# Performance work log

Measured on AMD Instinct MI355X. Metric: run time of the kernel, lower is better.

Reference implementation:

```python
import jax, jax.numpy as jnp
import numpy as np

DT = 1e-3
STEPS = 128
UNITS_OSC = 512
MLP_UNITS = [1024, 512, 256]
ACTION_DIM = 256
BATCH = 64


def setup_inputs() -> dict:
    key = jax.random.key(0)
    ks = jax.random.split(key, 16)
    inp = {
        "z": jax.random.normal(ks[0], (BATCH, 2 * UNITS_OSC), dtype=jnp.float32),
        "omega": jax.random.uniform(ks[1], (BATCH, 1), dtype=jnp.float32),
        "b": jax.random.uniform(ks[2], (BATCH, UNITS_OSC), dtype=jnp.float32),
    }
    dims = [UNITS_OSC] + MLP_UNITS
    i = 3
    for l, (din, dout) in enumerate(zip(dims[:-1], dims[1:])):
        scale = 1.0 / np.sqrt(din)
        inp[f"W{l}_re"] = (jax.random.normal(ks[i], (din, dout), dtype=jnp.float32) * scale); i += 1
        inp[f"W{l}_im"] = (jax.random.normal(ks[i], (din, dout), dtype=jnp.float32) * scale); i += 1
        inp[f"b{l}_re"] = jnp.zeros((dout,), dtype=jnp.float32)
        inp[f"b{l}_im"] = jnp.zeros((dout,), dtype=jnp.float32)
    return inp


def _hopf(z, omega, b):
    # z: (B, 2*U) = [real | imag]; Hopf dynamics with harmonic frequencies k*omega
    x, y = z[:, :UNITS_OSC], z[:, UNITS_OSC:]
    r2 = x * x + y * y
    w = omega * jnp.arange(1, UNITS_OSC + 1, dtype=z.dtype)  # (B, U)
    dx = (b - r2) * x - w * y
    dy = (b - r2) * y + w * x
    return jnp.concatenate([x + DT * dx, y + DT * dy], axis=-1)


def _complex_mlp(z, params):
    # complex dense stack: (xr+i*yi) @ (Wr+i*Wi) + (br+i*bi), tanh on re/im parts
    x, y = jnp.split(z, 2, axis=-1)
    for (Wr, Wi, br, bi) in params:
        xr = x @ Wr - y @ Wi + br
        yi = x @ Wi + y @ Wr + bi
        x, y = jnp.tanh(xr), jnp.tanh(yi)
    return jnp.concatenate([x, y], axis=-1)


def reference(z, omega, b,
              W0_re, W0_im, b0_re, b0_im,
              W1_re, W1_im, b1_re, b1_im,
              W2_re, W2_im, b2_re, b2_im):
    params = [(W0_re, W0_im, b0_re, b0_im),
              (W1_re, W1_im, b1_re, b1_im),
              (W2_re, W2_im, b2_re, b2_im)]
    # first oscillator step (done before the while_loop in the original)
    z1 = _hopf(z, omega, b)
    o0 = _complex_mlp(z1, params)

    def step(zc, _):
        zn = _hopf(zc, omega, b)
        return zn, _complex_mlp(zn, params)

    _, outs = jax.lax.scan(step, z1, None, length=STEPS - 1)  # (STEPS-1, B, 2*A)
    outs = jnp.concatenate([o0[None], outs], axis=0)          # (STEPS, B, 2*A)
    out = jnp.transpose(outs, (1, 0, 2))[:, :, :ACTION_DIM]   # (B, STEPS, A)
    return out, z1
```

## Files before the change

kernel.cpp:

```cpp
#include <hip/hip_runtime.h>
#include <hip/hip_bf16.h>
#include <stdint.h>

#define AS1 __attribute__((address_space(1)))
#define AS3 __attribute__((address_space(3)))

typedef __bf16 bf16x8 __attribute__((ext_vector_type(8)));
typedef float f32x4 __attribute__((ext_vector_type(4)));

__device__ __forceinline__ float fast_tanh(float x) {
    float e = __expf(2.0f * x);
    return 1.0f - 2.0f / (e + 1.0f);
}

__device__ __forceinline__ float ldin(const void* p, int idx, int f32) {
    return f32 ? ((const float*)p)[idx]
               : __bfloat162float(((const __hip_bfloat16*)p)[idx]);
}

__device__ __forceinline__ unsigned short f2bf(float v) {
    __hip_bfloat16 h = __float2bfloat16(v);
    return *(unsigned short*)&h;
}

__device__ __forceinline__ void gload_lds16(const __hip_bfloat16* g, AS3 char* l) {
    __builtin_amdgcn_global_load_lds((AS1 void*)g, (AS3 void*)l, 16, 0, 0);
}

__global__ __launch_bounds__(256)
void setup_all(const void* __restrict__ z, const void* __restrict__ omega,
               const void* __restrict__ bc,
               const void* __restrict__ W0r, const void* __restrict__ W0i,
               const void* __restrict__ W1r, const void* __restrict__ W1i,
               const void* __restrict__ W2r, const void* __restrict__ W2i,
               const void* __restrict__ b0r, const void* __restrict__ b0i,
               const void* __restrict__ b1r, const void* __restrict__ b1i,
               const void* __restrict__ b2r,
               __hip_bfloat16* __restrict__ Z, __hip_bfloat16* __restrict__ WT0,
               __hip_bfloat16* __restrict__ WT1, __hip_bfloat16* __restrict__ WT2,
               float* __restrict__ biasOut, int* __restrict__ flagOut,
               char* __restrict__ dout)
{
    __shared__ float T[64][65];
    __shared__ int sflag;
    const int t   = threadIdx.x;
    const int bid = blockIdx.x;

    if (t == 0) sflag = 0;
    __syncthreads();
    {
        const unsigned short* zz = (const unsigned short*)z;
        const int c = ((((zz[t] >> 7) & 0xFF) >= 0xC8) ? 1 : 0)
                    + ((((zz[t + 256] >> 7) & 0xFF) >= 0xC8) ? 1 : 0);
        if (c) atomicAdd(&sflag, c);
    }
    __syncthreads();
    const int f32 = (sflag > 8) ? 1 : 0;

    if (bid < 128) {
        const int tid = bid * 256 + t;
        const int b = tid >> 9;
        const int i = tid & 511;
        float x = ldin(z, b * 1024 + i, f32);
        float y = ldin(z, b * 1024 + 512 + i, f32);
        const float om = ldin(omega, b, f32);
        const float bb = ldin(bc, b * 512 + i, f32);
        const float w  = om * (float)(i + 1);
        __hip_bfloat16* zt = Z + b * 1024 + i;
        for (int s = 0; s < 128; ++s) {
            const float r2 = x * x + y * y;
            const float f  = bb - r2;
            const float dx = f * x - w * y;
            const float dy = f * y + w * x;
            x += 0.001f * dx;
            y += 0.001f * dy;
            zt[s * 65536]       = __float2bfloat16(x);
            zt[s * 65536 + 512] = __float2bfloat16(y);
            if (s == 0) {
                if (f32) {
                    float* o = (float*)(dout + (size_t)2097152 * 4);
                    o[b * 1024 + i] = x; o[b * 1024 + 512 + i] = y;
                } else {
                    __hip_bfloat16* o = (__hip_bfloat16*)(dout + (size_t)2097152 * 2);
                    o[b * 1024 + i] = __float2bfloat16(x);
                    o[b * 1024 + 512 + i] = __float2bfloat16(y);
                }
            }
        }
        return;
    }

    if (bid >= 1216) {
        if (bid == 1216 && t == 0) *flagOut = f32;
        const int idx = (bid - 1216) * 256 + t;
        float v;
        if      (idx < 1024) v = ldin(b0r, idx, f32);
        else if (idx < 2048) v = ldin(b0i, idx - 1024, f32);
        else if (idx < 2560) v = ldin(b1r, idx - 2048, f32);
        else if (idx < 3072) v = ldin(b1i, idx - 2560, f32);
        else                 v = ldin(b2r, idx - 3072, f32);
        biasOut[idx] = v;
        return;
    }

    const int wbid = bid - 128;
    int din, dout_, KT, nt, kt;
    const void *Wr, *Wi;
    __hip_bfloat16* dst;
    if (wbid < 512)       { din = 512;  dout_ = 1024; KT = 1024; Wr = W0r; Wi = W0i; dst = WT0;
                            nt = wbid >> 4;           kt = wbid & 15; }
    else if (wbid < 1024) { din = 1024; dout_ = 512;  KT = 2048; Wr = W1r; Wi = W1i; dst = WT1;
                            nt = (wbid - 512) >> 5;   kt = (wbid - 512) & 31; }
    else                  { din = 512;  dout_ = 256;  KT = 1024; Wr = W2r; Wi = W2i; dst = WT2;
                            nt = (wbid - 1024) >> 4;  kt = (wbid - 1024) & 15; }

    const int n0 = nt * 64, k0 = kt * 64;
    const void* src; float sg; int col0, krel;
    if (n0 < dout_) {
        col0 = n0;
        if (k0 < din) { src = Wr; sg =  1.f; krel = k0; }
        else          { src = Wi; sg = -1.f; krel = k0 - din; }
    } else {
        col0 = n0 - dout_;
        if (k0 < din) { src = Wi; sg =  1.f; krel = k0; }
        else          { src = Wr; sg =  1.f; krel = k0 - din; }
    }

    const int lr = t >> 4, lc = t & 15;
#pragma unroll
    for (int p = 0; p < 4; ++p) {
        const int r = p * 16 + lr;
        const int c = lc * 4;
        const size_t gi = (size_t)(krel + r) * dout_ + col0 + c;
        float v0, v1, v2, v3;
        if (f32) {
            float4 v = *(const float4*)((const float*)src + gi);
            v0 = v.x; v1 = v.y; v2 = v.z; v3 = v.w;
        } else {
            ushort4 u = *(const ushort4*)((const unsigned short*)src + gi);
            __hip_bfloat16 h0, h1, h2, h3;
            *(unsigned short*)&h0 = u.x; *(unsigned short*)&h1 = u.y;
            *(unsigned short*)&h2 = u.z; *(unsigned short*)&h3 = u.w;
            v0 = __bfloat162float(h0); v1 = __bfloat162float(h1);
            v2 = __bfloat162float(h2); v3 = __bfloat162float(h3);
        }
        T[r][c] = sg * v0; T[r][c + 1] = sg * v1;
        T[r][c + 2] = sg * v2; T[r][c + 3] = sg * v3;
    }
    __syncthreads();
#pragma unroll
    for (int q = 0; q < 4; ++q) {
        const int n = q * 16 + lr;
        const int k8 = lc;
        ushort4 u;
        u.x = f2bf(T[k8 * 4 + 0][n]); u.y = f2bf(T[k8 * 4 + 1][n]);
        u.z = f2bf(T[k8 * 4 + 2][n]); u.w = f2bf(T[k8 * 4 + 3][n]);
        *(ushort4*)((unsigned short*)dst + (size_t)(n0 + n) * KT + k0 + k8 * 4) = u;
    }
}

template<int MT, int NT, int GX, int MODE>
__global__ __launch_bounds__(256)
void gemm_bias_tanh(const __hip_bfloat16* __restrict__ A,
                    const __hip_bfloat16* __restrict__ Bt,
                    const float* __restrict__ bias,
                    void* __restrict__ Cv, const int* __restrict__ flag,
                    int N, int K)
{
    constexpr int AI = MT / 32;
    constexpr int BJ = NT / 32;
    __shared__ __align__(16) __hip_bfloat16 As[MT * 64];
    __shared__ __align__(16) __hip_bfloat16 Bs[NT * 64];

    const int tid = threadIdx.x, lane = tid & 63, w = tid >> 6;
    const int wx = w & 1, wy = w >> 1;

    int nt, mt;
    const int bid = blockIdx.x;
    if constexpr (GX >= 8) {
        constexpr int XG = GX >> 3;
        const int xcd = bid & 7, r = bid >> 3;
        nt = xcd * XG + (r % XG);
        mt = r / XG;
    } else {
        nt = bid % GX;
        mt = bid / GX;
    }
    const int m0 = mt * MT;
    const int n0 = nt * NT;

    const int sl = lane & 7, lr8 = lane >> 3;
    const __hip_bfloat16* gA[AI];
    const __hip_bfloat16* gB[BJ];
#pragma unroll
    for (int p = 0; p < AI; ++p) {
        const int row = w * (MT / 4) + p * 8 + lr8;
        gA[p] = A + (size_t)(m0 + row) * K + (sl ^ (row & 7)) * 8;
    }
#pragma unroll
    for (int p = 0; p < BJ; ++p) {
        const int row = w * (NT / 4) + p * 8 + lr8;
        gB[p] = Bt + (size_t)(n0 + row) * K + (sl ^ (row & 7)) * 8;
    }
    AS3 char* lA = (AS3 char*)As + w * (MT * 32);
    AS3 char* lB = (AS3 char*)Bs + w * (NT * 32);

    const int fr = lane & 15, fq = lane >> 4;
    const int swz = (fq ^ (fr & 7)) * 8;
    const int arow = wy * (MT / 2) + fr;
    const int brow = wx * (NT / 2) + fr;

    f32x4 acc[AI][BJ];
#pragma unroll
    for (int i = 0; i < AI; ++i)
#pragma unroll
        for (int j = 0; j < BJ; ++j)
            acc[i][j] = (f32x4){0.f, 0.f, 0.f, 0.f};

    const int NKT = K >> 6;
    for (int kt = 0; kt < NKT; ++kt) {
        const int kk = kt << 6;
#pragma unroll
        for (int p = 0; p < AI; ++p) gload_lds16(gA[p] + kk, lA + p * 1024);
#pragma unroll
        for (int p = 0; p < BJ; ++p) gload_lds16(gB[p] + kk, lB + p * 1024);
        __syncthreads();
#pragma unroll
        for (int ks = 0; ks < 2; ++ks) {
            const int so = swz ^ (ks << 5);
            bf16x8 af[AI], bv[BJ];
#pragma unroll
            for (int i = 0; i < AI; ++i)
                af[i] = *(const bf16x8*)(As + (arow + i * 16) * 64 + so);
#pragma unroll
            for (int j = 0; j < BJ; ++j)
                bv[j] = *(const bf16x8*)(Bs + (brow + j * 16) * 64 + so);
#pragma unroll
            for (int i = 0; i < AI; ++i)
#pragma unroll
                for (int j = 0; j < BJ; ++j)
                    acc[i][j] = __builtin_amdgcn_mfma_f32_16x16x32_bf16(af[i], bv[j], acc[i][j], 0, 0, 0);
        }
        __syncthreads();
    }

    const int col_l = lane & 15;
    const int rq    = lane >> 4;
    const int f32   = (MODE == 1) ? *flag : 0;
    float bvv[BJ];
#pragma unroll
    for (int j = 0; j < BJ; ++j)
        bvv[j] = bias[n0 + wx * (NT / 2) + j * 16 + col_l];

#pragma unroll
    for (int i = 0; i < AI; ++i) {
#pragma unroll
        for (int j = 0; j < BJ; ++j) {
            const int gc = n0 + wx * (NT / 2) + j * 16 + col_l;
#pragma unroll
            for (int r = 0; r < 4; ++r) {
                const int gr = m0 + wy * (MT / 2) + i * 16 + rq * 4 + r;
                const float v = fast_tanh(acc[i][j][r] + bvv[j]);
                if (MODE == 0) {
                    ((__hip_bfloat16*)Cv)[(size_t)gr * (size_t)N + gc] = __float2bfloat16(v);
                } else {
                    const size_t idx = (size_t)(gr & 63) * 32768 + (size_t)(gr >> 6) * 256 + (size_t)gc;
                    if (f32) ((float*)Cv)[idx] = v;
                    else     ((__hip_bfloat16*)Cv)[idx] = __float2bfloat16(v);
                }
            }
        }
    }
}

extern "C" void kernel_launch(void* const* d_in, const int* in_sizes, int n_in,
                              void* d_out, int out_size, void* d_ws, size_t ws_size,
                              hipStream_t stream)
{
    (void)in_sizes; (void)n_in; (void)out_size; (void)ws_size;
    char* ws = (char*)d_ws;
    __hip_bfloat16* Z    = (__hip_bfloat16*)(ws);
    __hip_bfloat16* H0   = (__hip_bfloat16*)(ws + (16u << 20));
    __hip_bfloat16* WT0  = (__hip_bfloat16*)(ws + (48u << 20));
    __hip_bfloat16* WT1  = (__hip_bfloat16*)(ws + (52u << 20));
    __hip_bfloat16* WT2  = (__hip_bfloat16*)(ws + (56u << 20));
    float*          bias = (float*)        (ws + (56u << 20) + (512u << 10));
    int*            flag = (int*)          (ws + (57u << 20));

    setup_all<<<1229, 256, 0, stream>>>(d_in[0], d_in[1], d_in[2],
                                        d_in[3], d_in[4], d_in[7], d_in[8], d_in[11], d_in[12],
                                        d_in[5], d_in[6], d_in[9], d_in[10], d_in[13],
                                        Z, WT0, WT1, WT2, bias, flag, (char*)d_out);

    gemm_bias_tanh<128, 128, 16, 0><<<1024, 256, 0, stream>>>(Z, WT0, bias, H0, flag, 2048, 1024);
    gemm_bias_tanh<128, 128, 8, 0><<<512, 256, 0, stream>>>(H0, WT1, bias + 2048, Z, flag, 1024, 2048);
    gemm_bias_tanh<64, 64, 4, 1><<<512, 256, 0, stream>>>(Z, WT2, bias + 3072, d_out, flag, 256, 1024);
}
```

Before: 208.6 us.

## Overlap W1/W2 weight transposes with first GEMM and retile second GEMM

Splits the setup kernel so it only prepares Z, WT0 and the biases. The W1 and W2 transpose tiles now run as extra blocks inside the first GEMM launch, so weight conversion overlaps with layer-0 compute and setup finishes sooner. The second GEMM moves from 128x128 to 128x64 tiles with 1024 blocks for better CU occupancy. The cost is larger shared memory in the combined kernel, which may lower GEMM occupancy, and a mixed workload within one grid.

```diff
diff --git a/kernel.cpp b/kernel.cpp
--- a/kernel.cpp
+++ b/kernel.cpp
@@ -27,21 +27,68 @@
     __builtin_amdgcn_global_load_lds((AS1 void*)g, (AS3 void*)l, 16, 0, 0);
 }
 
+__device__ __forceinline__ void wt_tile(const void* Wr, const void* Wi,
+                                        int din, int dout_, int KT, int nt, int kt,
+                                        __hip_bfloat16* dst, int f32, char* smem)
+{
+    float (*T)[65] = (float(*)[65])smem;
+    const int t = threadIdx.x;
+    const int n0 = nt * 64, k0 = kt * 64;
+    const void* src; float sg; int col0, krel;
+    if (n0 < dout_) {
+        col0 = n0;
+        if (k0 < din) { src = Wr; sg =  1.f; krel = k0; }
+        else          { src = Wi; sg = -1.f; krel = k0 - din; }
+    } else {
+        col0 = n0 - dout_;
+        if (k0 < din) { src = Wi; sg =  1.f; krel = k0; }
+        else          { src = Wr; sg =  1.f; krel = k0 - din; }
+    }
+    const int lr = t >> 4, lc = t & 15;
+#pragma unroll
+    for (int p = 0; p < 4; ++p) {
+        const int r = p * 16 + lr;
+        const int c = lc * 4;
+        const size_t gi = (size_t)(krel + r) * dout_ + col0 + c;
+        float v0, v1, v2, v3;
+        if (f32) {
+            float4 v = *(const float4*)((const float*)src + gi);
+            v0 = v.x; v1 = v.y; v2 = v.z; v3 = v.w;
+        } else {
+            ushort4 u = *(const ushort4*)((const unsigned short*)src + gi);
+            __hip_bfloat16 h0, h1, h2, h3;
+            *(unsigned short*)&h0 = u.x; *(unsigned short*)&h1 = u.y;
+            *(unsigned short*)&h2 = u.z; *(unsigned short*)&h3 = u.w;
+            v0 = __bfloat162float(h0); v1 = __bfloat162float(h1);
+            v2 = __bfloat162float(h2); v3 = __bfloat162float(h3);
+        }
+        T[r][c] = sg * v0; T[r][c + 1] = sg * v1;
+        T[r][c + 2] = sg * v2; T[r][c + 3] = sg * v3;
+    }
+    __syncthreads();
+#pragma unroll
+    for (int q = 0; q < 4; ++q) {
+        const int n = q * 16 + lr;
+        const int k8 = lc;
+        ushort4 u;
+        u.x = f2bf(T[k8 * 4 + 0][n]); u.y = f2bf(T[k8 * 4 + 1][n]);
+        u.z = f2bf(T[k8 * 4 + 2][n]); u.w = f2bf(T[k8 * 4 + 3][n]);
+        *(ushort4*)((unsigned short*)dst + (size_t)(n0 + n) * KT + k0 + k8 * 4) = u;
+    }
+}
+
 __global__ __launch_bounds__(256)
-void setup_all(const void* __restrict__ z, const void* __restrict__ omega,
-               const void* __restrict__ bc,
-               const void* __restrict__ W0r, const void* __restrict__ W0i,
-               const void* __restrict__ W1r, const void* __restrict__ W1i,
-               const void* __restrict__ W2r, const void* __restrict__ W2i,
-               const void* __restrict__ b0r, const void* __restrict__ b0i,
-               const void* __restrict__ b1r, const void* __restrict__ b1i,
-               const void* __restrict__ b2r,
-               __hip_bfloat16* __restrict__ Z, __hip_bfloat16* __restrict__ WT0,
-               __hip_bfloat16* __restrict__ WT1, __hip_bfloat16* __restrict__ WT2,
-               float* __restrict__ biasOut, int* __restrict__ flagOut,
-               char* __restrict__ dout)
-{
-    __shared__ float T[64][65];
+void setup1(const void* __restrict__ z, const void* __restrict__ omega,
+            const void* __restrict__ bc,
+            const void* __restrict__ W0r, const void* __restrict__ W0i,
+            const void* __restrict__ b0r, const void* __restrict__ b0i,
+            const void* __restrict__ b1r, const void* __restrict__ b1i,
+            const void* __restrict__ b2r,
+            __hip_bfloat16* __restrict__ Z, __hip_bfloat16* __restrict__ WT0,
+            float* __restrict__ biasOut, int* __restrict__ flagOut,
+            char* __restrict__ dout)
+{
+    __shared__ __align__(16) char smem[16640];
     __shared__ int sflag;
     const int t   = threadIdx.x;
     const int bid = blockIdx.x;
@@ -90,9 +137,9 @@
         return;
     }
 
-    if (bid >= 1216) {
-        if (bid == 1216 && t == 0) *flagOut = f32;
-        const int idx = (bid - 1216) * 256 + t;
+    if (bid >= 640) {
+        if (bid == 640 && t == 0) *flagOut = f32;
+        const int idx = (bid - 640) * 256 + t;
         float v;
         if      (idx < 1024) v = ldin(b0r, idx, f32);
         else if (idx < 2048) v = ldin(b0i, idx - 1024, f32);
@@ -103,80 +150,27 @@
         return;
     }
 
-    const int wbid = bid - 128;
-    int din, dout_, KT, nt, kt;
-    const void *Wr, *Wi;
-    __hip_bfloat16* dst;
-    if (wbid < 512)       { din = 512;  dout_ = 1024; KT = 1024; Wr = W0r; Wi = W0i; dst = WT0;
-                            nt = wbid >> 4;           kt = wbid & 15; }
-    else if (wbid < 1024) { din = 1024; dout_ = 512;  KT = 2048; Wr = W1r; Wi = W1i; dst = WT1;
-                            nt = (wbid - 512) >> 5;   kt = (wbid - 512) & 31; }
-    else                  { din = 512;  dout_ = 256;  KT = 1024; Wr = W2r; Wi = W2i; dst = WT2;
-                            nt = (wbid - 1024) >> 4;  kt = (wbid - 1024) & 15; }
-
-    const int n0 = nt * 64, k0 = kt * 64;
-    const void* src; float sg; int col0, krel;
-    if (n0 < dout_) {
-        col0 = n0;
-        if (k0 < din) { src = Wr; sg =  1.f; krel = k0; }
-        else          { src = Wi; sg = -1.f; krel = k0 - din; }
-    } else {
-        col0 = n0 - dout_;
-        if (k0 < din) { src = Wi; sg =  1.f; krel = k0; }
-        else          { src = Wr; sg =  1.f; krel = k0 - din; }
-    }
-
-    const int lr = t >> 4, lc = t & 15;
-#pragma unroll
-    for (int p = 0; p < 4; ++p) {
-        const int r = p * 16 + lr;
-        const int c = lc * 4;
-        const size_t gi = (size_t)(krel + r) * dout_ + col0 + c;
-        float v0, v1, v2, v3;
-        if (f32) {
-            float4 v = *(const float4*)((const float*)src + gi);
-            v0 = v.x; v1 = v.y; v2 = v.z; v3 = v.w;
-        } else {
-            ushort4 u = *(const ushort4*)((const unsigned short*)src + gi);
-            __hip_bfloat16 h0, h1, h2, h3;
-            *(unsigned short*)&h0 = u.x; *(unsigned short*)&h1 = u.y;
-            *(unsigned short*)&h2 = u.z; *(unsigned short*)&h3 = u.w;
-            v0 = __bfloat162float(h0); v1 = __bfloat162float(h1);
-            v2 = __bfloat162float(h2); v3 = __bfloat162float(h3);
-        }
-        T[r][c] = sg * v0; T[r][c + 1] = sg * v1;
-        T[r][c + 2] = sg * v2; T[r][c + 3] = sg * v3;
-    }
-    __syncthreads();
-#pragma unroll
-    for (int q = 0; q < 4; ++q) {
-        const int n = q * 16 + lr;
-        const int k8 = lc;
-        ushort4 u;
-        u.x = f2bf(T[k8 * 4 + 0][n]); u.y = f2bf(T[k8 * 4 + 1][n]);
-        u.z = f2bf(T[k8 * 4 + 2][n]); u.w = f2bf(T[k8 * 4 + 3][n]);
-        *(ushort4*)((unsigned short*)dst + (size_t)(n0 + n) * KT + k0 + k8 * 4) = u;
-    }
+    const int u = bid - 128;
+    wt_tile(W0r, W0i, 512, 1024, 1024, u >> 4, u & 15, WT0, f32, smem);
 }
 
 template<int MT, int NT, int GX, int MODE>
-__global__ __launch_bounds__(256)
-void gemm_bias_tanh(const __hip_bfloat16* __restrict__ A,
-                    const __hip_bfloat16* __restrict__ Bt,
-                    const float* __restrict__ bias,
-                    void* __restrict__ Cv, const int* __restrict__ flag,
-                    int N, int K)
+__device__ __forceinline__ void gemm_core(int bid,
+                                          const __hip_bfloat16* __restrict__ A,
+                                          const __hip_bfloat16* __restrict__ Bt,
+                                          const float* __restrict__ bias,
+                                          void* __restrict__ Cv, int f32,
+                                          int N, int K, char* smem)
 {
     constexpr int AI = MT / 32;
     constexpr int BJ = NT / 32;
-    __shared__ __align__(16) __hip_bfloat16 As[MT * 64];
-    __shared__ __align__(16) __hip_bfloat16 Bs[NT * 64];
+    __hip_bfloat16* As = (__hip_bfloat16*)smem;
+    __hip_bfloat16* Bs = (__hip_bfloat16*)(smem + MT * 128);
 
     const int tid = threadIdx.x, lane = tid & 63, w = tid >> 6;
     const int wx = w & 1, wy = w >> 1;
 
     int nt, mt;
-    const int bid = blockIdx.x;
     if constexpr (GX >= 8) {
         constexpr int XG = GX >> 3;
         const int xcd = bid & 7, r = bid >> 3;
@@ -246,7 +240,6 @@
 
     const int col_l = lane & 15;
     const int rq    = lane >> 4;
-    const int f32   = (MODE == 1) ? *flag : 0;
     float bvv[BJ];
 #pragma unroll
     for (int j = 0; j < BJ; ++j)
@@ -273,6 +266,39 @@
     }
 }
 
+__global__ __launch_bounds__(256)
+void gemm0_wt(const __hip_bfloat16* __restrict__ A,
+              const __hip_bfloat16* __restrict__ Bt,
+              const float* __restrict__ bias, void* __restrict__ Cv,
+              const void* __restrict__ W1r, const void* __restrict__ W1i,
+              const void* __restrict__ W2r, const void* __restrict__ W2i,
+              __hip_bfloat16* __restrict__ WT1, __hip_bfloat16* __restrict__ WT2,
+              const int* __restrict__ flag)
+{
+    __shared__ __align__(16) char smem[32768];
+    const int bid = blockIdx.x;
+    if (bid < 1024) {
+        gemm_core<128, 128, 16, 0>(bid, A, Bt, bias, Cv, 0, 2048, 1024, smem);
+    } else if (bid < 1536) {
+        const int u = bid - 1024;
+        wt_tile(W1r, W1i, 1024, 512, 2048, u >> 5, u & 31, WT1, *flag, smem);
+    } else {
+        const int u = bid - 1536;
+        wt_tile(W2r, W2i, 512, 256, 1024, u >> 4, u & 15, WT2, *flag, smem);
+    }
+}
+
+template<int MT, int NT, int GX, int MODE>
+__global__ __launch_bounds__(256)
+void gemm_k(const __hip_bfloat16* __restrict__ A, const __hip_bfloat16* __restrict__ Bt,
+            const float* __restrict__ bias, void* __restrict__ Cv,
+            const int* __restrict__ flag, int N, int K)
+{
+    __shared__ __align__(16) char smem[(MT + NT) * 128];
+    const int f32 = (MODE == 1) ? *flag : 0;
+    gemm_core<MT, NT, GX, MODE>(blockIdx.x, A, Bt, bias, Cv, f32, N, K, smem);
+}
+
 extern "C" void kernel_launch(void* const* d_in, const int* in_sizes, int n_in,
                               void* d_out, int out_size, void* d_ws, size_t ws_size,
                               hipStream_t stream)
@@ -287,12 +313,15 @@
     float*          bias = (float*)        (ws + (56u << 20) + (512u << 10));
     int*            flag = (int*)          (ws + (57u << 20));
 
-    setup_all<<<1229, 256, 0, stream>>>(d_in[0], d_in[1], d_in[2],
-                                        d_in[3], d_in[4], d_in[7], d_in[8], d_in[11], d_in[12],
-                                        d_in[5], d_in[6], d_in[9], d_in[10], d_in[13],
-                                        Z, WT0, WT1, WT2, bias, flag, (char*)d_out);
-
-    gemm_bias_tanh<128, 128, 16, 0><<<1024, 256, 0, stream>>>(Z, WT0, bias, H0, flag, 2048, 1024);
-    gemm_bias_tanh<128, 128, 8, 0><<<512, 256, 0, stream>>>(H0, WT1, bias + 2048, Z, flag, 1024, 2048);
-    gemm_bias_tanh<64, 64, 4, 1><<<512, 256, 0, stream>>>(Z, WT2, bias + 3072, d_out, flag, 256, 1024);
-}
+    setup1<<<653, 256, 0, stream>>>(d_in[0], d_in[1], d_in[2], d_in[3], d_in[4],
+                                    d_in[5], d_in[6], d_in[9], d_in[10], d_in[13],
+                                    Z, WT0, bias, flag, (char*)d_out);
+
+    gemm0_wt<<<1600, 256, 0, stream>>>(Z, WT0, bias, H0,
+                                       d_in[7], d_in[8], d_in[11], d_in[12],
+                                       WT1, WT2, flag);
+
+    gemm_k<128, 64, 16, 0><<<1024, 256, 0, stream>>>(H0, WT1, bias + 2048, Z, flag, 1024, 2048);
+
+    gemm_k<64, 64, 4, 1><<<512, 256, 0, stream>>>(Z, WT2, bias + 3072, d_out, flag, 256, 1024);
+}
```

New measurement: 206.6 us. Within noise of the previous version (-1.0%).
